# Kernel tuning notes

Hardware: AMD Instinct MI355X
Metric: run time of the kernel (lower is better)

The kernel has to match this reference:

```python
import jax, jax.numpy as jnp
import numpy as np

B, P, M, C = 8, 131072, 16, 2
THRESHOLD = 0.5
GAMMA = 2.0
ALPHA_W = 0.25  # focal 'weight' for the foreground class


def _cxcycz_to_xyz(b):
    return jnp.concatenate([b[..., :3] - b[..., 3:] / 2, b[..., :3] + b[..., 3:] / 2], -1)


def _xyz_to_cxcycz(b):
    return jnp.concatenate([(b[..., :3] + b[..., 3:]) / 2, b[..., 3:] - b[..., :3]], -1)


def _encode(cxcycz, priors_cxcycz):
    # standard SSD encoding with variances (10, 5), extended to 3D
    return jnp.concatenate([
        (cxcycz[..., :3] - priors_cxcycz[..., :3]) / (priors_cxcycz[..., 3:] / 10.0),
        jnp.log(cxcycz[..., 3:] / priors_cxcycz[..., 3:]) * 5.0], -1)


def _jaccard3d(a, b):
    # a: [M,6] xyz boxes, b: [P,6] xyz boxes -> [M,P] IoU
    lo = jnp.maximum(a[:, None, :3], b[None, :, :3])
    hi = jnp.minimum(a[:, None, 3:], b[None, :, 3:])
    inter = jnp.prod(jnp.clip(hi - lo, 0.0, None), -1)
    va = jnp.prod(a[:, 3:] - a[:, :3], -1)
    vb = jnp.prod(b[:, 3:] - b[:, :3], -1)
    return inter / (va[:, None] + vb[None, :] - inter)


def setup_inputs():
    key = jax.random.key(0)
    k1, k2, k3, k4, k5, k6 = jax.random.split(key, 6)
    predicted_locs = jax.random.normal(k1, (B, P, 6), jnp.float32)
    predicted_scores = jax.random.normal(k2, (B, P, C), jnp.float32)
    # valid ground-truth boxes in boundary (xyz) coords inside unit cube
    ctr = jax.random.uniform(k3, (B, M, 3)) * 0.8 + 0.1
    sz = jax.random.uniform(k4, (B, M, 3)) * 0.15 + 0.05
    boxes = jnp.concatenate([ctr - sz / 2, ctr + sz / 2], -1)
    # priors in center-size (cxcycz) coords
    pctr = jax.random.uniform(k5, (P, 3)) * 0.9 + 0.05
    psz = jax.random.uniform(k6, (P, 3)) * 0.2 + 0.03
    priors_cxcycz = jnp.concatenate([pctr, psz], -1)
    labels = jnp.ones((B, M), jnp.int32)  # single foreground class
    return dict(predicted_locs=predicted_locs, predicted_scores=predicted_scores,
                boxes=boxes, labels=labels, priors_cxcycz=priors_cxcycz)


def _forward(predicted_locs, predicted_scores, boxes, priors_cxcycz, labels):
    priors_xyz = _cxcycz_to_xyz(priors_cxcycz)

    def match(boxes_i, labels_i):
        ov = _jaccard3d(boxes_i, priors_xyz)           # [M, P]
        overlap_fep = ov.max(0)                        # [P] best IoU per prior
        object_fep = ov.argmax(0)                      # [P] best object per prior
        prior_feo = ov.argmax(1)                       # [M] best prior per object
        # force each object to own its best prior
        object_fep = object_fep.at[prior_feo].set(jnp.arange(M))
        overlap_fep = overlap_fep.at[prior_feo].set(1.0)
        lab = labels_i[object_fep]
        lab = jnp.where(overlap_fep < THRESHOLD, 0, lab)  # hard thresholding
        tl = _encode(_xyz_to_cxcycz(boxes_i[object_fep]), priors_cxcycz)
        return lab, tl

    true_classes, true_locs = jax.vmap(match)(boxes, labels)  # [B,P], [B,P,6]

    pos = true_classes > 0
    n_pos = pos.sum()
    # nn.L1Loss() = mean over all selected elements (n_pos priors x 6 coords)
    diff = jnp.abs(predicted_locs - true_locs) * pos[..., None].astype(predicted_locs.dtype)
    loc_loss = jnp.where(n_pos > 0,
                         diff.sum() / jnp.maximum(n_pos.astype(jnp.float32) * 6.0, 1.0),
                         jnp.float32(0.0))

    # sigmoid focal loss on foreground channel (include_background=False, C==2)
    x = predicted_scores[..., 1]                       # [B,P] fg logit
    t = pos.astype(x.dtype)
    ce = -(t * jax.nn.log_sigmoid(x) + (1.0 - t) * jax.nn.log_sigmoid(-x))
    p = jax.nn.sigmoid(x)
    pt = jnp.where(pos, p, 1.0 - p)
    focal = (ALPHA_W * t + (1.0 - ALPHA_W) * (1.0 - t)) * (1.0 - pt) ** GAMMA * ce
    conf_loss = focal.mean()
    return conf_loss, loc_loss


def reference(predicted_locs, predicted_scores, boxes, labels, priors_cxcycz):
    return _forward(predicted_locs, predicted_scores, boxes, priors_cxcycz, labels)
```

## Files before the change

### kernel.cpp

```cpp
#include <hip/hip_runtime.h>

#define NB 8
#define NP 131072
#define NM 16
#define THRESH 0.5f
#define BLK 256
#define PPT 4
#define PPB (BLK * PPT)
#define BPB (NP / PPB)
#define NPAIR (NB * NM)
#define NBLOCKS (NB * BPB)

typedef unsigned long long u64;
typedef unsigned int u32;


template <int CTRL>
__device__ __forceinline__ float dppmv(float x) {
    return __int_as_float(__builtin_amdgcn_update_dpp(
        0, __float_as_int(x), CTRL, 0xf, 0xf, false));
}

__device__ __forceinline__ float wave_max63(float x) {
    x = fmaxf(x, dppmv<0x111>(x));
    x = fmaxf(x, dppmv<0x112>(x));
    x = fmaxf(x, dppmv<0x114>(x));
    x = fmaxf(x, dppmv<0x118>(x));
    x = fmaxf(x, dppmv<0x142>(x));
    x = fmaxf(x, dppmv<0x143>(x));
    return x;
}

__device__ __forceinline__ float wave_sum63(float x) {
    x += dppmv<0x111>(x);
    x += dppmv<0x112>(x);
    x += dppmv<0x114>(x);
    x += dppmv<0x118>(x);
    x += dppmv<0x142>(x);
    x += dppmv<0x143>(x);
    return x;
}

__device__ __forceinline__ float bcast63(float x) {
    return __int_as_float(__builtin_amdgcn_readlane(__float_as_int(x), 63));
}


__device__ __forceinline__ float iou_term(float inter, float va, float vb) {
    return (inter > 0.0f) ? inter * __builtin_amdgcn_rcpf(va + vb - inter) : 0.0f;
}

__device__ __forceinline__ float iou_box(const float4 A, const float4 B4,
                                         const float pl[3], const float ph[3],
                                         float vb) {
    float d0 = fminf(A.w,  ph[0]) - fmaxf(A.x, pl[0]);
    float d1 = fminf(B4.x, ph[1]) - fmaxf(A.y, pl[1]);
    float d2 = fminf(B4.y, ph[2]) - fmaxf(A.z, pl[2]);
    float inter = fmaxf(d0, 0.0f) * fmaxf(d1, 0.0f) * fmaxf(d2, 0.0f);
    return iou_term(inter, B4.z, vb);
}

__device__ __forceinline__ float focal_term(float x, bool pos) {
    float t = __expf(-fabsf(x));
    float r = __builtin_amdgcn_rcpf(1.0f + t);
    float L = __logf(1.0f + t);
    float ce = (pos ? fmaxf(-x, 0.0f) : fmaxf(x, 0.0f)) + L;
    float omp = (pos == (x >= 0.0f)) ? t * r : r;
    float w = pos ? 0.25f : 0.75f;
    return w * omp * omp * ce;
}

__device__ __forceinline__ float l1_enc(const float* lp,
                                        const float blo[3], const float bhi[3],
                                        const float pc[3], const float ps[3]) {
    float s = 0.0f;
#pragma unroll
    for (int k = 0; k < 3; ++k) {
        float gc = (blo[k] + bhi[k]) / 2.0f;
        float gs = bhi[k] - blo[k];
        float e  = (gc - pc[k]) / (ps[k] / 10.0f);
        float e2 = __logf(gs / ps[k]) * 5.0f;
        s += fabsf(lp[k]     - e);
        s += fabsf(lp[3 + k] - e2);
    }
    return s;
}

__device__ __forceinline__ u32 decode_p(u64 k) { return ~(u32)(k & 0xFFFFFFFFull); }


__global__ __launch_bounds__(BLK) void match_loss_kernel(
        const float* __restrict__ locs, const float* __restrict__ scores,
        const float* __restrict__ boxes, const int* __restrict__ labels,
        const float* __restrict__ priors,
        u64* __restrict__ keys_out,
        float4* __restrict__ part) {
    __shared__ float4 s_box[NM][2];
    __shared__ u64    s_wkey[4][NM];
    __shared__ float  s_wred[4][3];

    const int tid  = threadIdx.x;
    const int b    = blockIdx.y;
    const int lane = tid & 63, wave = tid >> 6;
    const int p0   = blockIdx.x * PPB + PPT * tid;

    if (tid < NM) {
        const float* bx = &boxes[(b * NM + tid) * 6];
        float l0 = bx[0], l1 = bx[1], l2 = bx[2];
        float h0 = bx[3], h1 = bx[4], h2 = bx[5];
        s_box[tid][0] = make_float4(l0, l1, l2, h0);
        float va = (h0 - l0) * (h1 - l1) * (h2 - l2);
        s_box[tid][1] = make_float4(h1, h2, va, __int_as_float(labels[b * NM + tid]));
    }
    __syncthreads();

    const float4* pr4 = reinterpret_cast<const float4*>(priors);
    const size_t f4b = (size_t)(p0 / 2) * 3;
    float4 q0 = pr4[f4b + 0], q1 = pr4[f4b + 1], q2 = pr4[f4b + 2];
    float4 q3 = pr4[f4b + 3], q4 = pr4[f4b + 4], q5 = pr4[f4b + 5];
    float pl[PPT][3], ph[PPT][3], vb[PPT];
    {
        const float qf[24] = {q0.x,q0.y,q0.z,q0.w, q1.x,q1.y,q1.z,q1.w,
                              q2.x,q2.y,q2.z,q2.w, q3.x,q3.y,q3.z,q3.w,
                              q4.x,q4.y,q4.z,q4.w, q5.x,q5.y,q5.z,q5.w};
#pragma unroll
        for (int j = 0; j < PPT; ++j) {
#pragma unroll
            for (int k = 0; k < 3; ++k) {
                float c = qf[6 * j + k], s = qf[6 * j + 3 + k];
                pl[j][k] = c - s / 2.0f;
                ph[j][k] = c + s / 2.0f;
            }
            vb[j] = (ph[j][0] - pl[j][0]) * (ph[j][1] - pl[j][1]) * (ph[j][2] - pl[j][2]);
        }
    }

    float ci[NM]; u32 cp[NM];
    float best[PPT]; int bm[PPT];
#pragma unroll
    for (int j = 0; j < PPT; ++j) { best[j] = -1.0f; bm[j] = 0; }
#pragma unroll
    for (int m = 0; m < NM; ++m) {
        float4 A = s_box[m][0], B4 = s_box[m][1];
        float i0 = iou_box(A, B4, pl[0], ph[0], vb[0]);
        float i1 = iou_box(A, B4, pl[1], ph[1], vb[1]);
        float i2 = iou_box(A, B4, pl[2], ph[2], vb[2]);
        float i3 = iou_box(A, B4, pl[3], ph[3], vb[3]);
        if (i0 > best[0]) { best[0] = i0; bm[0] = m; }
        if (i1 > best[1]) { best[1] = i1; bm[1] = m; }
        if (i2 > best[2]) { best[2] = i2; bm[2] = m; }
        if (i3 > best[3]) { best[3] = i3; bm[3] = m; }
        float v = i0; u32 w = (u32)p0;
        if (i1 > v) { v = i1; w = (u32)(p0 + 1); }
        if (i2 > v) { v = i2; w = (u32)(p0 + 2); }
        if (i3 > v) { v = i3; w = (u32)(p0 + 3); }
        ci[m] = v; cp[m] = w;
    }

#pragma unroll
    for (int m = 0; m < NM; ++m) {
        float wm = bcast63(wave_max63(ci[m]));
        u64 eq = __ballot(ci[m] == wm);
        int ls = __ffsll(eq) - 1;
        u32 wp = (u32)__builtin_amdgcn_readlane((int)cp[m], ls);
        if (lane == 0)
            s_wkey[wave][m] = ((u64)__float_as_uint(wm) << 32) | (u32)~wp;
    }

    const float4* sc4 = reinterpret_cast<const float4*>(scores);
    const size_t scb = ((size_t)b * NP + p0) >> 1;
    float4 sA = sc4[scb], sB = sc4[scb + 1];
    const float xs[PPT] = {sA.y, sA.w, sB.y, sB.w};

    float f = 0.0f, l = 0.0f, n = 0.0f;
#pragma unroll
    for (int j = 0; j < PPT; ++j) {
        float4 Bb = s_box[bm[j]][1];
        const bool pos = (best[j] >= THRESH) && (__float_as_int(Bb.w) > 0);
        f += focal_term(xs[j], pos);
        if (pos) {
            const int p = p0 + j;
            float pc[3], ps[3];
#pragma unroll
            for (int k = 0; k < 3; ++k) { pc[k] = priors[p * 6 + k]; ps[k] = priors[p * 6 + 3 + k]; }
            float4 Ab = s_box[bm[j]][0];
            float blo[3] = {Ab.x, Ab.y, Ab.z}, bhi[3] = {Ab.w, Bb.x, Bb.y};
            l += l1_enc(&locs[((size_t)b * NP + p) * 6], blo, bhi, pc, ps);
            n += 1.0f;
        }
    }

    f = wave_sum63(f); l = wave_sum63(l); n = wave_sum63(n);
    if (lane == 63) { s_wred[wave][0] = f; s_wred[wave][1] = l; s_wred[wave][2] = n; }
    __syncthreads();

    if (tid < NM) {
        u64 k = s_wkey[0][tid];
#pragma unroll
        for (int w = 1; w < 4; ++w) k = (s_wkey[w][tid] > k) ? s_wkey[w][tid] : k;
        keys_out[(size_t)(b * NM + tid) * BPB + blockIdx.x] = k;
    }
    if (tid == 0) {
        part[b * BPB + blockIdx.x] =
            make_float4(s_wred[0][0] + s_wred[1][0] + s_wred[2][0] + s_wred[3][0],
                        s_wred[0][1] + s_wred[1][1] + s_wred[2][1] + s_wred[3][1],
                        s_wred[0][2] + s_wred[1][2] + s_wred[2][2] + s_wred[3][2],
                        0.0f);
    }
}


__global__ __launch_bounds__(1024) void finalize_kernel(
        const float* __restrict__ locs, const float* __restrict__ scores,
        const float* __restrict__ boxes, const int* __restrict__ labels,
        const float* __restrict__ priors, const u64* __restrict__ keys_in,
        const float4* __restrict__ part, float* __restrict__ out) {
    __shared__ u64   s_key[NPAIR];
    __shared__ float s_red[16][3];
    __shared__ float s_fix[16][3];
    const int t = threadIdx.x, lane = t & 63, wave = t >> 6;

    float f = 0.0f, l = 0.0f, n = 0.0f;
    for (int i = t; i < NBLOCKS; i += 1024) {
        float4 v = part[i]; f += v.x; l += v.y; n += v.z;
    }
    f = wave_sum63(f); l = wave_sum63(l); n = wave_sum63(n);
    if (lane == 63) { s_red[wave][0] = f; s_red[wave][1] = l; s_red[wave][2] = n; }

#pragma unroll
    for (int i = 0; i < 8; ++i) {
        const int pair = wave * 8 + i;
        const u64* kp = keys_in + (size_t)pair * BPB;
        u64 k = 0;
#pragma unroll
        for (int j = 0; j < BPB / 64; ++j) {
            u64 v = kp[j * 64 + lane];
            k = (v > k) ? v : k;
        }
#pragma unroll
        for (int off = 32; off > 0; off >>= 1) {
            u64 o = __shfl_down(k, off);
            k = (o > k) ? o : k;
        }
        if (lane == 0) s_key[pair] = k;
    }
    __syncthreads();

    float df = 0.0f, dl = 0.0f, dn = 0.0f;
    if (t < NPAIR) {
        const int b = t / NM, m = t % NM;
        const u32 pstar = decode_p(s_key[t]);
        bool skip = false;
        for (int mm = m + 1; mm < NM; ++mm)
            skip |= (decode_p(s_key[b * NM + mm]) == pstar);
        if (!skip) {
            const int p = (int)pstar;
            float pc[3], ps[3], pl[3], ph[3];
#pragma unroll
            for (int k = 0; k < 3; ++k) { pc[k] = priors[p * 6 + k]; ps[k] = priors[p * 6 + 3 + k]; }
#pragma unroll
            for (int k = 0; k < 3; ++k) { pl[k] = pc[k] - ps[k] / 2.0f; ph[k] = pc[k] + ps[k] / 2.0f; }
            const float vb = (ph[0] - pl[0]) * (ph[1] - pl[1]) * (ph[2] - pl[2]);

            float best = -1.0f; int bestm = 0;
            for (int mm = 0; mm < NM; ++mm) {
                const float* bx = &boxes[(b * NM + mm) * 6];
                float d0 = fminf(bx[3], ph[0]) - fmaxf(bx[0], pl[0]);
                float d1 = fminf(bx[4], ph[1]) - fmaxf(bx[1], pl[1]);
                float d2 = fminf(bx[5], ph[2]) - fmaxf(bx[2], pl[2]);
                float inter = fmaxf(d0, 0.0f) * fmaxf(d1, 0.0f) * fmaxf(d2, 0.0f);
                float va = (bx[3] - bx[0]) * (bx[4] - bx[1]) * (bx[5] - bx[2]);
                float iou = iou_term(inter, va, vb);
                if (iou > best) { best = iou; bestm = mm; }
            }
            const bool old_pos = (best >= THRESH) && (labels[b * NM + bestm] > 0);
            const bool new_pos = (labels[b * NM + m] > 0);

            const float x = scores[((size_t)b * NP + p) * 2 + 1];
            df = focal_term(x, new_pos) - focal_term(x, old_pos);
            dn = (new_pos ? 1.0f : 0.0f) - (old_pos ? 1.0f : 0.0f);

            const float* lp = &locs[((size_t)b * NP + p) * 6];
            if (new_pos) {
                const float* bx = &boxes[(b * NM + m) * 6];
                float blo[3] = {bx[0], bx[1], bx[2]}, bhi[3] = {bx[3], bx[4], bx[5]};
                dl += l1_enc(lp, blo, bhi, pc, ps);
            }
            if (old_pos) {
                const float* bx = &boxes[(b * NM + bestm) * 6];
                float blo[3] = {bx[0], bx[1], bx[2]}, bhi[3] = {bx[3], bx[4], bx[5]};
                dl -= l1_enc(lp, blo, bhi, pc, ps);
            }
        }
    }
    df = wave_sum63(df); dl = wave_sum63(dl); dn = wave_sum63(dn);
    if (lane == 63) { s_fix[wave][0] = df; s_fix[wave][1] = dl; s_fix[wave][2] = dn; }
    __syncthreads();

    if (t == 0) {
        float tf = 0.0f, tl = 0.0f, tn = 0.0f;
        for (int w = 0; w < 16; ++w) {
            tf += s_red[w][0] + s_fix[w][0];
            tl += s_red[w][1] + s_fix[w][1];
            tn += s_red[w][2] + s_fix[w][2];
        }
        out[0] = tf / (float)(NB * NP);
        out[1] = (tn > 0.5f) ? tl / fmaxf(tn * 6.0f, 1.0f) : 0.0f;
    }
}


extern "C" void kernel_launch(void* const* d_in, const int* in_sizes, int n_in,
                              void* d_out, int out_size, void* d_ws, size_t ws_size,
                              hipStream_t stream) {
    const float* locs   = (const float*)d_in[0];
    const float* scores = (const float*)d_in[1];
    const float* boxes  = (const float*)d_in[2];
    const int*   labels = (const int*)d_in[3];
    const float* priors = (const float*)d_in[4];
    float* out = (float*)d_out;

    u64*    keys = (u64*)d_ws;
    float4* part = (float4*)((char*)d_ws + (size_t)NPAIR * BPB * 8);

    dim3 grid(BPB, NB);
    match_loss_kernel<<<grid, BLK, 0, stream>>>(locs, scores, boxes, labels, priors,
                                                keys, part);
    finalize_kernel<<<1, 1024, 0, stream>>>(locs, scores, boxes, labels, priors, keys,
                                            part, out);
}
```

Before: 34.48 us.

## Fuse finalize into match kernel via last-block counter and atomicMax keys

Drops the separate finalize kernel launch. Each block now reduces its per-pair keys with a global 64-bit atomicMax instead of writing per-block keys, and the last block to arrive, found through an atomic counter with threadfences, does the final reduction and the fixup. This adds a memset of the workspace before the launch and puts the tail work on a single 256-thread block. It also adds atomic contention on 128 addresses across 1024 blocks.

```diff
diff --git a/kernel.cpp b/kernel.cpp
--- a/kernel.cpp
+++ b/kernel.cpp
@@ -93,11 +93,16 @@
         const float* __restrict__ locs, const float* __restrict__ scores,
         const float* __restrict__ boxes, const int* __restrict__ labels,
         const float* __restrict__ priors,
-        u64* __restrict__ keys_out,
-        float4* __restrict__ part) {
+        u64* __restrict__ keys,
+        u32* __restrict__ counter,
+        float4* __restrict__ part,
+        float* __restrict__ out) {
     __shared__ float4 s_box[NM][2];
     __shared__ u64    s_wkey[4][NM];
     __shared__ float  s_wred[4][3];
+    __shared__ u64    s_key[NPAIR];
+    __shared__ float  s_red[4][3], s_fix[4][3];
+    __shared__ u32    s_last;
 
     const int tid  = threadIdx.x;
     const int b    = blockIdx.y;
@@ -198,7 +203,7 @@
         u64 k = s_wkey[0][tid];
 #pragma unroll
         for (int w = 1; w < 4; ++w) k = (s_wkey[w][tid] > k) ? s_wkey[w][tid] : k;
-        keys_out[(size_t)(b * NM + tid) * BPB + blockIdx.x] = k;
+        atomicMax(&keys[b * NM + tid], k);
     }
     if (tid == 0) {
         part[b * BPB + blockIdx.x] =
@@ -207,87 +212,69 @@
                         s_wred[0][2] + s_wred[1][2] + s_wred[2][2] + s_wred[3][2],
                         0.0f);
     }
-}
-
-
-__global__ __launch_bounds__(1024) void finalize_kernel(
-        const float* __restrict__ locs, const float* __restrict__ scores,
-        const float* __restrict__ boxes, const int* __restrict__ labels,
-        const float* __restrict__ priors, const u64* __restrict__ keys_in,
-        const float4* __restrict__ part, float* __restrict__ out) {
-    __shared__ u64   s_key[NPAIR];
-    __shared__ float s_red[16][3];
-    __shared__ float s_fix[16][3];
-    const int t = threadIdx.x, lane = t & 63, wave = t >> 6;
-
-    float f = 0.0f, l = 0.0f, n = 0.0f;
-    for (int i = t; i < NBLOCKS; i += 1024) {
-        float4 v = part[i]; f += v.x; l += v.y; n += v.z;
-    }
-    f = wave_sum63(f); l = wave_sum63(l); n = wave_sum63(n);
-    if (lane == 63) { s_red[wave][0] = f; s_red[wave][1] = l; s_red[wave][2] = n; }
-
-#pragma unroll
-    for (int i = 0; i < 8; ++i) {
-        const int pair = wave * 8 + i;
-        const u64* kp = keys_in + (size_t)pair * BPB;
-        u64 k = 0;
-#pragma unroll
-        for (int j = 0; j < BPB / 64; ++j) {
-            u64 v = kp[j * 64 + lane];
-            k = (v > k) ? v : k;
-        }
-#pragma unroll
-        for (int off = 32; off > 0; off >>= 1) {
-            u64 o = __shfl_down(k, off);
-            k = (o > k) ? o : k;
-        }
-        if (lane == 0) s_key[pair] = k;
-    }
+    __syncthreads();
+
+    if (tid == 0) {
+        __threadfence();
+        s_last = (atomicAdd(counter, 1u) == (u32)(NBLOCKS - 1)) ? 1u : 0u;
+    }
+    __syncthreads();
+    if (!s_last) return;
+
+    __threadfence();
+
+    float rf = 0.0f, rl = 0.0f, rn = 0.0f;
+    for (int i = tid; i < NBLOCKS; i += BLK) {
+        float4 v = part[i]; rf += v.x; rl += v.y; rn += v.z;
+    }
+    rf = wave_sum63(rf); rl = wave_sum63(rl); rn = wave_sum63(rn);
+    if (lane == 63) { s_red[wave][0] = rf; s_red[wave][1] = rl; s_red[wave][2] = rn; }
+
+    if (tid < NPAIR) s_key[tid] = keys[tid];
     __syncthreads();
 
     float df = 0.0f, dl = 0.0f, dn = 0.0f;
-    if (t < NPAIR) {
-        const int b = t / NM, m = t % NM;
-        const u32 pstar = decode_p(s_key[t]);
+    if (tid < NPAIR) {
+        const int bb = tid / NM, m = tid % NM;
+        const u32 pstar = decode_p(s_key[tid]);
         bool skip = false;
         for (int mm = m + 1; mm < NM; ++mm)
-            skip |= (decode_p(s_key[b * NM + mm]) == pstar);
+            skip |= (decode_p(s_key[bb * NM + mm]) == pstar);
         if (!skip) {
             const int p = (int)pstar;
-            float pc[3], ps[3], pl[3], ph[3];
+            float pc[3], ps[3], fl[3], fh[3];
 #pragma unroll
             for (int k = 0; k < 3; ++k) { pc[k] = priors[p * 6 + k]; ps[k] = priors[p * 6 + 3 + k]; }
 #pragma unroll
-            for (int k = 0; k < 3; ++k) { pl[k] = pc[k] - ps[k] / 2.0f; ph[k] = pc[k] + ps[k] / 2.0f; }
-            const float vb = (ph[0] - pl[0]) * (ph[1] - pl[1]) * (ph[2] - pl[2]);
-
-            float best = -1.0f; int bestm = 0;
+            for (int k = 0; k < 3; ++k) { fl[k] = pc[k] - ps[k] / 2.0f; fh[k] = pc[k] + ps[k] / 2.0f; }
+            const float fvb = (fh[0] - fl[0]) * (fh[1] - fl[1]) * (fh[2] - fl[2]);
+
+            float fbest = -1.0f; int fbm = 0;
             for (int mm = 0; mm < NM; ++mm) {
-                const float* bx = &boxes[(b * NM + mm) * 6];
-                float d0 = fminf(bx[3], ph[0]) - fmaxf(bx[0], pl[0]);
-                float d1 = fminf(bx[4], ph[1]) - fmaxf(bx[1], pl[1]);
-                float d2 = fminf(bx[5], ph[2]) - fmaxf(bx[2], pl[2]);
+                const float* bx = &boxes[(bb * NM + mm) * 6];
+                float d0 = fminf(bx[3], fh[0]) - fmaxf(bx[0], fl[0]);
+                float d1 = fminf(bx[4], fh[1]) - fmaxf(bx[1], fl[1]);
+                float d2 = fminf(bx[5], fh[2]) - fmaxf(bx[2], fl[2]);
                 float inter = fmaxf(d0, 0.0f) * fmaxf(d1, 0.0f) * fmaxf(d2, 0.0f);
                 float va = (bx[3] - bx[0]) * (bx[4] - bx[1]) * (bx[5] - bx[2]);
-                float iou = iou_term(inter, va, vb);
-                if (iou > best) { best = iou; bestm = mm; }
+                float iou = iou_term(inter, va, fvb);
+                if (iou > fbest) { fbest = iou; fbm = mm; }
             }
-            const bool old_pos = (best >= THRESH) && (labels[b * NM + bestm] > 0);
-            const bool new_pos = (labels[b * NM + m] > 0);
-
-            const float x = scores[((size_t)b * NP + p) * 2 + 1];
+            const bool old_pos = (fbest >= THRESH) && (labels[bb * NM + fbm] > 0);
+            const bool new_pos = (labels[bb * NM + m] > 0);
+
+            const float x = scores[((size_t)bb * NP + p) * 2 + 1];
             df = focal_term(x, new_pos) - focal_term(x, old_pos);
             dn = (new_pos ? 1.0f : 0.0f) - (old_pos ? 1.0f : 0.0f);
 
-            const float* lp = &locs[((size_t)b * NP + p) * 6];
+            const float* lp = &locs[((size_t)bb * NP + p) * 6];
             if (new_pos) {
-                const float* bx = &boxes[(b * NM + m) * 6];
+                const float* bx = &boxes[(bb * NM + m) * 6];
                 float blo[3] = {bx[0], bx[1], bx[2]}, bhi[3] = {bx[3], bx[4], bx[5]};
                 dl += l1_enc(lp, blo, bhi, pc, ps);
             }
             if (old_pos) {
-                const float* bx = &boxes[(b * NM + bestm) * 6];
+                const float* bx = &boxes[(bb * NM + fbm) * 6];
                 float blo[3] = {bx[0], bx[1], bx[2]}, bhi[3] = {bx[3], bx[4], bx[5]};
                 dl -= l1_enc(lp, blo, bhi, pc, ps);
             }
@@ -297,9 +284,9 @@
     if (lane == 63) { s_fix[wave][0] = df; s_fix[wave][1] = dl; s_fix[wave][2] = dn; }
     __syncthreads();
 
-    if (t == 0) {
+    if (tid == 0) {
         float tf = 0.0f, tl = 0.0f, tn = 0.0f;
-        for (int w = 0; w < 16; ++w) {
+        for (int w = 0; w < 4; ++w) {
             tf += s_red[w][0] + s_fix[w][0];
             tl += s_red[w][1] + s_fix[w][1];
             tn += s_red[w][2] + s_fix[w][2];
@@ -320,12 +307,13 @@
     const float* priors = (const float*)d_in[4];
     float* out = (float*)d_out;
 
-    u64*    keys = (u64*)d_ws;
-    float4* part = (float4*)((char*)d_ws + (size_t)NPAIR * BPB * 8);
+    u64*    keys    = (u64*)d_ws;
+    u32*    counter = (u32*)((char*)d_ws + 1024);
+    float4* part    = (float4*)((char*)d_ws + 2048);
+
+    hipMemsetAsync(d_ws, 0, 2048, stream);
 
     dim3 grid(BPB, NB);
     match_loss_kernel<<<grid, BLK, 0, stream>>>(locs, scores, boxes, labels, priors,
-                                                keys, part);
-    finalize_kernel<<<1, 1024, 0, stream>>>(locs, scores, boxes, labels, priors, keys,
-                                            part, out);
-}
+                                                keys, counter, part, out);
+}
```

Measured after the change: 44.23 us. 1.28x slower.
